# Kernel optimization log

Measured on AMD Instinct MI355X. Metric: run time of the kernel, lower is better.

The kernel has to match this reference:

```python
import jax, jax.numpy as jnp
import numpy as np

N_NODES = 50000
N_EDGES = 800000
IN_DIM = 13
HID = 64
LAYER_DIMS = [(IN_DIM, HID), (HID, HID), (HID, HID), (HID, HID), (HID, 1)]


def setup_inputs() -> dict:
    key = jax.random.key(0)
    ks = jax.random.split(key, 20)
    x = jax.random.normal(ks[0], (N_NODES, IN_DIM), dtype=jnp.float32)
    edge_index = jax.random.randint(ks[1], (2, N_EDGES), 0, N_NODES)
    edge_weight = jax.random.uniform(ks[2], (N_EDGES,), dtype=jnp.float32)
    inp = {"x": x, "edge_index": edge_index, "edge_weight": edge_weight}
    for i, (di, do) in enumerate(LAYER_DIMS):
        s = 1.0 / np.sqrt(di)
        inp[f"Wrel{i}"] = (jax.random.normal(ks[3 + 3 * i], (di, do)) * s).astype(jnp.float32)
        inp[f"brel{i}"] = jnp.zeros((do,), dtype=jnp.float32)
        inp[f"Wroot{i}"] = (jax.random.normal(ks[4 + 3 * i], (di, do)) * s).astype(jnp.float32)
    return inp


def _graph_conv(x, src, dst, ew, Wrel, brel, Wroot):
    # PyG GraphConv: out = lin_rel(sum_{j in N(i)} w_e * x_j) + lin_root(x_i)
    msgs = ew[:, None] * x[src]                      # [E, d_in] gather
    aggr = jax.ops.segment_sum(msgs, dst, num_segments=N_NODES)  # [N, d_in]
    return aggr @ Wrel + brel + x @ Wroot


def reference(x, edge_index, edge_weight,
              Wrel0, brel0, Wroot0,
              Wrel1, brel1, Wroot1,
              Wrel2, brel2, Wroot2,
              Wrel3, brel3, Wroot3,
              Wrel4, brel4, Wroot4):
    src, dst = edge_index[0], edge_index[1]  # source_to_target flow
    params = [
        (Wrel0, brel0, Wroot0),
        (Wrel1, brel1, Wroot1),
        (Wrel2, brel2, Wroot2),
        (Wrel3, brel3, Wroot3),
        (Wrel4, brel4, Wroot4),
    ]
    h = x
    for Wr, br, Ws in params[:-1]:
        h = jax.nn.relu(_graph_conv(h, src, dst, edge_weight, Wr, br, Ws))
    Wr, br, Ws = params[-1]
    h = _graph_conv(h, src, dst, edge_weight, Wr, br, Ws)
    return jax.nn.sigmoid(h)  # [N, 1]
```

## Files before the change

kernel.cpp:

```cpp
#include <hip/hip_runtime.h>
#include <math.h>

#define N_NODES 50000
#define N_EDGES 800000
#define NBUCKET 196
#define CHUNK 4096
#define NCHUNK 196
#define SCAN_N (NBUCKET * NCHUNK)
#define SB_A 151
#define SB_B 196
#define EPT 16
#define CAP_FINE 8192
#define MAXEPAD (N_EDGES + N_NODES * 4)

typedef __attribute__((ext_vector_type(8))) _Float16 f16x8;
typedef __attribute__((ext_vector_type(4))) float f32x4;

__device__ __forceinline__ int roundup4(int v) { return (v + 3) & ~3; }


__device__ __forceinline__ int block_excl_scan(int v, int* wsum) {
    int t = threadIdx.x, lane = t & 63, w = t >> 6;
    int sc = v;
    #pragma unroll
    for (int o = 1; o < 64; o <<= 1) {
        int u = __shfl_up(sc, o, 64);
        if (lane >= o) sc += u;
    }
    if (lane == 63) wsum[w] = sc;
    __syncthreads();
    int add = 0;
    #pragma unroll
    for (int j = 0; j < 4; ++j) if (j < w) add += wsum[j];
    return add + sc - v;
}


__global__ void hist_kernel(const int* __restrict__ dst, int* __restrict__ h,
                            int* __restrict__ counts) {
    __shared__ int hist[NBUCKET];
    for (int i = threadIdx.x; i < NBUCKET; i += 256) hist[i] = 0;
    __syncthreads();
    int base = blockIdx.x * CHUNK;
    int n = min(CHUNK, N_EDGES - base);
    for (int k = threadIdx.x; k < n; k += 256) {
        int d = dst[base + k];
        atomicAdd(&hist[d >> 8], 1);
        atomicAdd(&counts[d], 1);
    }
    __syncthreads();
    for (int i = threadIdx.x; i < NBUCKET; i += 256)
        h[i * NCHUNK + blockIdx.x] = hist[i];
}


__global__ void scan_blocks_dual(int* __restrict__ h, const int* __restrict__ counts,
                                 int* __restrict__ offs, int* __restrict__ blocksums) {
    __shared__ int wsum[4];
    int bid = blockIdx.x, t = threadIdx.x;
    if (bid < SB_A) {
        int i = bid * 256 + t;
        int v = (i < SCAN_N) ? h[i] : 0;
        int e = block_excl_scan(v, wsum);
        if (i < SCAN_N) h[i] = e;
        if (t == 255) blocksums[bid] = e + v;
    } else {
        int j = (bid - SB_A) * 256 + t;
        int v = (j < N_NODES) ? roundup4(counts[j]) : 0;
        int e = block_excl_scan(v, wsum);
        if (j < N_NODES) offs[j] = e;
        if (t == 255) blocksums[bid] = e + v;
    }
}

__global__ void scan_mid(const int* __restrict__ blocksums, int* __restrict__ blockoffs) {
    __shared__ int wsum[4];
    int base = (blockIdx.x == 0) ? 0 : SB_A;
    int n = (blockIdx.x == 0) ? SB_A : SB_B;
    int t = threadIdx.x;
    int v = (t < n) ? blocksums[base + t] : 0;
    int e = block_excl_scan(v, wsum);
    if (t < n) blockoffs[base + t] = e;
}

__global__ void scan_add_dual(int* __restrict__ h, int* __restrict__ offs,
                              const int* __restrict__ counts,
                              const int* __restrict__ blockoffs) {
    int bid = blockIdx.x, t = threadIdx.x;
    if (bid < SB_A) {
        int i = bid * 256 + t;
        if (i < SCAN_N) h[i] += blockoffs[bid];
    } else {
        int j = (bid - SB_A) * 256 + t;
        if (j < N_NODES) {
            int v = offs[j] + blockoffs[bid];
            offs[j] = v;
            if (j == N_NODES - 1) offs[N_NODES] = v + roundup4(counts[j]);
        }
    }
}


__launch_bounds__(256, 4)
__global__ void scatter_coarse(const int* __restrict__ src, const int* __restrict__ dst,
                               const float* __restrict__ ew, const int* __restrict__ hs,
                               int2* __restrict__ ecoarse) {
    __shared__ int cnt[NBUCKET];
    __shared__ int excl[NBUCKET];
    __shared__ int cur[NBUCKET];
    __shared__ int gbase[NBUCKET];
    __shared__ int wsum[4];
    __shared__ int2 stage[CHUNK];

    int t = threadIdx.x;
    int base = blockIdx.x * CHUNK;
    int n = min(CHUNK, N_EDGES - base);

    for (int i = t; i < NBUCKET; i += 256) {
        cnt[i] = 0;
        gbase[i] = hs[i * NCHUNK + blockIdx.x];
    }
    __syncthreads();

    int rx[EPT];
    float rw[EPT];
    #pragma unroll
    for (int j = 0; j < EPT; ++j) {
        int k = t + j * 256;
        if (k < n) {
            int e = base + k;
            int d = dst[e];
            rx[j] = (d << 16) | src[e];
            rw[j] = ew[e];
            atomicAdd(&cnt[d >> 8], 1);
        }
    }
    __syncthreads();

    {
        int v = (t < NBUCKET) ? cnt[t] : 0;
        int e = block_excl_scan(v, wsum);
        if (t < NBUCKET) { excl[t] = e; cur[t] = e; }
    }
    __syncthreads();

    #pragma unroll
    for (int j = 0; j < EPT; ++j) {
        int k = t + j * 256;
        if (k < n) {
            int b = ((unsigned)rx[j]) >> 24;
            int p = atomicAdd(&cur[b], 1);
            stage[p] = make_int2(rx[j], __float_as_int(rw[j]));
        }
    }
    __syncthreads();

    for (int k = t; k < n; k += 256) {
        int2 r = stage[k];
        int b = ((unsigned)r.x) >> 24;
        ecoarse[gbase[b] + (k - excl[b])] = r;
    }
}


__launch_bounds__(256)
__global__ void fine_sort(const int* __restrict__ h, const int* __restrict__ offs,
                          const int2* __restrict__ ecoarse, int2* __restrict__ esrt) {
    int b = blockIdx.x, t = threadIdx.x;
    __shared__ int cur[256];
    __shared__ int2 stage[CAP_FINE];
    int bstartU = h[b * NCHUNK];
    int bendU = (b == NBUCKET - 1) ? N_EDGES : h[(b + 1) * NCHUNK];
    int nbU = bendU - bstartU;
    int P = offs[b << 8];
    int nodeEnd = min((b + 1) << 8, N_NODES);
    int plen = offs[nodeEnd] - P;
    int dstv = (b << 8) + t;
    cur[t] = (dstv < N_NODES) ? offs[dstv] - P : 0;
    __syncthreads();
    if (plen <= CAP_FINE) {
        for (int k = t; k < plen; k += 256) stage[k] = make_int2(0, 0);
        __syncthreads();
        for (int k = t; k < nbU; k += 256) {
            int2 r = ecoarse[bstartU + k];
            int d = (((unsigned)r.x) >> 16) & 255;
            int p = atomicAdd(&cur[d], 1);
            stage[p] = make_int2(r.x & 0xFFFF, r.y);
        }
        __syncthreads();
        for (int k = t; k < plen; k += 256) esrt[P + k] = stage[k];
    } else {
        for (int k = t; k < plen; k += 256) esrt[P + k] = make_int2(0, 0);
        __syncthreads();
        for (int k = t; k < nbU; k += 256) {
            int2 r = ecoarse[bstartU + k];
            int d = (((unsigned)r.x) >> 16) & 255;
            int p = atomicAdd(&cur[d], 1);
            esrt[P + p] = make_int2(r.x & 0xFFFF, r.y);
        }
    }
}


__global__ void wconv(const float* __restrict__ W1r, const float* __restrict__ W1o,
                      const float* __restrict__ W2r, const float* __restrict__ W2o,
                      const float* __restrict__ W3r, const float* __restrict__ W3o,
                      _Float16* __restrict__ wfrag) {
    int b = blockIdx.x, t = threadIdx.x;
    const float* Wr = (b == 0) ? W1r : (b == 1) ? W2r : W3r;
    const float* Wo = (b == 0) ? W1o : (b == 1) ? W2o : W3o;
    _Float16* out = wfrag + (size_t)b * 8192;
    for (int i = t; i < 1024; i += 256) {
        int frag = i >> 6, lane = i & 63;
        int m = frag >> 3, ct = (frag >> 1) & 3, ks = frag & 1;
        int col = ct * 16 + (lane & 15);
        int kb = ks * 32 + (lane >> 4) * 8;
        const float* W = m ? Wo : Wr;
        f16x8 v;
        #pragma unroll
        for (int j = 0; j < 8; ++j) v[j] = (_Float16)W[(kb + j) * 64 + col];
        *(f16x8*)&out[(size_t)i * 8] = v;
    }
}


__device__ __forceinline__ float bcast(float v, int k) {
    return __int_as_float(__builtin_amdgcn_readlane(__float_as_int(v), k));
}


__launch_bounds__(256)
__global__ void layer0_fused(const int* __restrict__ offs, const int2* __restrict__ esrt,
                             const float* __restrict__ x, const float* __restrict__ Wrel,
                             const float* __restrict__ bias, const float* __restrict__ Wroot,
                             _Float16* __restrict__ h0) {
    int wid = (blockIdx.x * blockDim.x + threadIdx.x) >> 6;
    int lane = threadIdx.x & 63;
    float wr[13], wo[13];
    #pragma unroll
    for (int k = 0; k < 13; ++k) {
        wr[k] = Wrel[k * 64 + lane];
        wo[k] = Wroot[k * 64 + lane];
    }
    float bc = bias[lane];
    int q = lane >> 4, f = lane & 15;
    int beg = offs[wid], end = offs[wid + 1];
    float acc = 0.f;
    bool fv = (f < 13);
    int i = beg + q;
    for (; i + 4 < end; i += 8) {
        int2 e0 = esrt[i], e1 = esrt[i + 4];
        float v0 = fv ? x[(size_t)e0.x * 13 + f] : 0.f;
        float v1 = fv ? x[(size_t)e1.x * 13 + f] : 0.f;
        acc = fmaf(__int_as_float(e0.y), v0, acc);
        acc = fmaf(__int_as_float(e1.y), v1, acc);
    }
    if (i < end) {
        int2 e = esrt[i];
        float v = fv ? x[(size_t)e.x * 13 + f] : 0.f;
        acc = fmaf(__int_as_float(e.y), v, acc);
    }
    acc += __shfl_xor(acc, 16, 64);
    acc += __shfl_xor(acc, 32, 64);
    float hv = (lane < 13) ? x[(size_t)wid * 13 + lane] : 0.f;
    float a0 = bc, a1 = 0.f, a2 = 0.f, a3 = 0.f;
    #pragma unroll
    for (int k = 0; k + 2 <= 13; k += 2) {
        a0 = fmaf(bcast(acc, k), wr[k], a0);
        a1 = fmaf(bcast(hv, k), wo[k], a1);
        a2 = fmaf(bcast(acc, k + 1), wr[k + 1], a2);
        a3 = fmaf(bcast(hv, k + 1), wo[k + 1], a3);
    }
    a0 = fmaf(bcast(acc, 12), wr[12], a0);
    a1 = fmaf(bcast(hv, 12), wo[12], a1);
    float o = fmaxf((a0 + a2) + (a1 + a3), 0.f);
    h0[(size_t)wid * 64 + lane] = (_Float16)o;
}


template <bool FINAL>
__launch_bounds__(256)
__global__ void layer_fused(const int* __restrict__ offs, const int2* __restrict__ esrt,
                            const _Float16* __restrict__ hin, const _Float16* __restrict__ wfrag_l,
                            const float* __restrict__ bias, _Float16* __restrict__ hout,
                            const float* __restrict__ Wrel4, const float* __restrict__ Wroot4,
                            float* __restrict__ z, float* __restrict__ root) {
    __shared__ __align__(16) _Float16 bfrag[16][64][8];
    __shared__ __align__(16) float aggrT[32][68];
    __shared__ __align__(16) _Float16 hrootT[32][72];
    __shared__ float zpart[4][32], rpart[4][32];
    int t = threadIdx.x;
    int rowbase = blockIdx.x * 32;

    {
        const int4* s = (const int4*)wfrag_l;
        int4* d = (int4*)&bfrag[0][0][0];
        #pragma unroll
        for (int i = 0; i < 4; ++i) d[t + 256 * i] = s[t + 256 * i];
    }
    {
        int row = t >> 3, c8 = (t & 7) * 8;
        int gr = min(rowbase + row, N_NODES - 1);
        *(int4*)&hrootT[row][c8] = *(const int4*)&hin[(size_t)gr * 64 + c8];
    }

    int qw = t >> 4, l = t & 15;
    int hi8 = l >> 3, f8 = l & 7;
    #pragma unroll
    for (int rr = 0; rr < 2; ++rr) {
        int node = rowbase + qw + rr * 16;
        float a[8] = {0.f, 0.f, 0.f, 0.f, 0.f, 0.f, 0.f, 0.f};
        if (node < N_NODES) {
            int beg = offs[node], end = offs[node + 1];
            for (int i = beg; i < end; i += 4) {
                int4 p0 = *(const int4*)(esrt + i);
                int4 p1 = *(const int4*)(esrt + i + 2);
                int s0 = hi8 ? p0.z : p0.x;
                int s1 = hi8 ? p1.z : p1.x;
                float w0 = __int_as_float(hi8 ? p0.w : p0.y);
                float w1 = __int_as_float(hi8 ? p1.w : p1.y);
                f16x8 r0 = *(const f16x8*)(hin + (size_t)s0 * 64 + f8 * 8);
                f16x8 r1 = *(const f16x8*)(hin + (size_t)s1 * 64 + f8 * 8);
                #pragma unroll
                for (int j = 0; j < 8; ++j) {
                    a[j] = fmaf(w0, (float)r0[j], a[j]);
                    a[j] = fmaf(w1, (float)r1[j], a[j]);
                }
            }
        }
        #pragma unroll
        for (int j = 0; j < 8; ++j) a[j] += __shfl_xor(a[j], 8, 64);
        float4 wv = make_float4(a[hi8 * 4 + 0], a[hi8 * 4 + 1], a[hi8 * 4 + 2], a[hi8 * 4 + 3]);
        *(float4*)&aggrT[qw + rr * 16][f8 * 8 + hi8 * 4] = wv;
    }
    __syncthreads();

    int w = t >> 6, lane = t & 63;
    int r = lane & 15, koff = (lane >> 4) * 8;
    float bc = bias[w * 16 + r];
    float w4rv = 0.f, w4ov = 0.f;
    if (FINAL) { w4rv = Wrel4[w * 16 + r]; w4ov = Wroot4[w * 16 + r]; }

    #pragma unroll
    for (int g = 0; g < 2; ++g) {
        int lr = g * 16 + r;
        f16x8 Ah[2], Al[2], Ar[2];
        #pragma unroll
        for (int ks = 0; ks < 2; ++ks) {
            float4 a0 = *(const float4*)&aggrT[lr][ks * 32 + koff];
            float4 a1 = *(const float4*)&aggrT[lr][ks * 32 + koff + 4];
            float vv[8] = {a0.x, a0.y, a0.z, a0.w, a1.x, a1.y, a1.z, a1.w};
            f16x8 hi, lo;
            #pragma unroll
            for (int j = 0; j < 8; ++j) {
                _Float16 hh = (_Float16)vv[j];
                hi[j] = hh;
                lo[j] = (_Float16)(vv[j] - (float)hh);
            }
            Ah[ks] = hi;
            Al[ks] = lo;
            Ar[ks] = *(const f16x8*)&hrootT[lr][ks * 32 + koff];
        }
        f32x4 acc = {bc, bc, bc, bc};
        #pragma unroll
        for (int ks = 0; ks < 2; ++ks) {
            f16x8 br = *(const f16x8*)&bfrag[(0 * 4 + w) * 2 + ks][lane][0];
            f16x8 bo = *(const f16x8*)&bfrag[(1 * 4 + w) * 2 + ks][lane][0];
            acc = __builtin_amdgcn_mfma_f32_16x16x32_f16(Ah[ks], br, acc, 0, 0, 0);
            acc = __builtin_amdgcn_mfma_f32_16x16x32_f16(Al[ks], br, acc, 0, 0, 0);
            acc = __builtin_amdgcn_mfma_f32_16x16x32_f16(Ar[ks], bo, acc, 0, 0, 0);
        }
        if (FINAL) {
            #pragma unroll
            for (int j = 0; j < 4; ++j) {
                float o = fmaxf(acc[j], 0.f);
                float zz = o * w4rv, rv = o * w4ov;
                #pragma unroll
                for (int m = 1; m < 16; m <<= 1) {
                    zz += __shfl_xor(zz, m, 64);
                    rv += __shfl_xor(rv, m, 64);
                }
                if (r == 0) {
                    int lrow = g * 16 + (lane >> 4) * 4 + j;
                    zpart[w][lrow] = zz;
                    rpart[w][lrow] = rv;
                }
            }
        } else {
            #pragma unroll
            for (int j = 0; j < 4; ++j) {
                int row = rowbase + g * 16 + (lane >> 4) * 4 + j;
                if (row < N_NODES)
                    hout[(size_t)row * 64 + w * 16 + r] = (_Float16)fmaxf(acc[j], 0.f);
            }
        }
    }
    if (FINAL) {
        __syncthreads();
        if (t < 32) {
            int row = rowbase + t;
            if (row < N_NODES) {
                z[row] = zpart[0][t] + zpart[1][t] + zpart[2][t] + zpart[3][t];
                root[row] = rpart[0][t] + rpart[1][t] + rpart[2][t] + rpart[3][t];
            }
        }
    }
}


__launch_bounds__(256)
__global__ void final_aggr(const int* __restrict__ offs, const int2* __restrict__ esrt,
                           const float* __restrict__ z, const float* __restrict__ root,
                           const float* __restrict__ b4, float* __restrict__ out) {
    int tid = blockIdx.x * blockDim.x + threadIdx.x;
    int node = tid >> 2, g = tid & 3;
    if (node >= N_NODES) return;
    int beg = offs[node], end = offs[node + 1];
    float a = 0.f;
    int i = beg + g;
    for (; i + 4 < end; i += 8) {
        int2 e0 = esrt[i], e1 = esrt[i + 4];
        a = fmaf(__int_as_float(e0.y), z[e0.x], a);
        a = fmaf(__int_as_float(e1.y), z[e1.x], a);
    }
    if (i < end) {
        int2 e = esrt[i];
        a = fmaf(__int_as_float(e.y), z[e.x], a);
    }
    a += __shfl_xor(a, 1, 64);
    a += __shfl_xor(a, 2, 64);
    if (g == 0) {
        float v = a + b4[0] + root[node];
        out[node] = 1.f / (1.f + expf(-v));
    }
}


extern "C" void kernel_launch(void* const* d_in, const int* in_sizes, int n_in,
                              void* d_out, int out_size, void* d_ws, size_t ws_size,
                              hipStream_t stream) {
    const float* x = (const float*)d_in[0];
    const int* eidx = (const int*)d_in[1];
    const float* ew = (const float*)d_in[2];
    const float* Wrel[5];
    const float* brel[5];
    const float* Wroot[5];
    for (int i = 0; i < 5; ++i) {
        Wrel[i] = (const float*)d_in[3 + 3 * i];
        brel[i] = (const float*)d_in[4 + 3 * i];
        Wroot[i] = (const float*)d_in[5 + 3 * i];
    }
    const int* src = eidx;
    const int* dst = eidx + N_EDGES;
    float* out = (float*)d_out;

    char* ws = (char*)d_ws;
    size_t off = 0;
    auto alloc = [&](size_t bytes) -> void* {
        void* p = ws + off;
        off = (off + bytes + 255) & ~(size_t)255;
        return p;
    };
    int* h = (int*)alloc((size_t)(SCAN_N + 256) * 4);
    int* blocksums = (int*)alloc(512 * 4);
    int* blockoffs = (int*)alloc(512 * 4);
    int* counts = (int*)alloc((size_t)N_NODES * 4);
    int* offs = (int*)alloc((size_t)(N_NODES + 1) * 4);
    int2* esrt = (int2*)alloc((size_t)MAXEPAD * 8);
    _Float16* h0 = (_Float16*)alloc((size_t)N_NODES * 64 * 2);
    _Float16* h1 = (_Float16*)alloc((size_t)N_NODES * 64 * 2);
    _Float16* wfrag = (_Float16*)alloc((size_t)3 * 8192 * 2);
    float* z = (float*)alloc((size_t)N_NODES * 4);
    float* root = (float*)alloc((size_t)N_NODES * 4);
    int2* ecoarse = (int2*)h0;
    (void)ws_size; (void)in_sizes; (void)n_in; (void)out_size;

    hipMemsetAsync(counts, 0, (size_t)N_NODES * 4, stream);
    hist_kernel<<<NCHUNK, 256, 0, stream>>>(dst, h, counts);
    scan_blocks_dual<<<SB_A + SB_B, 256, 0, stream>>>(h, counts, offs, blocksums);
    scan_mid<<<2, 256, 0, stream>>>(blocksums, blockoffs);
    scan_add_dual<<<SB_A + SB_B, 256, 0, stream>>>(h, offs, counts, blockoffs);
    scatter_coarse<<<NCHUNK, 256, 0, stream>>>(src, dst, ew, h, ecoarse);
    fine_sort<<<NBUCKET, 256, 0, stream>>>(h, offs, ecoarse, esrt);

    wconv<<<3, 256, 0, stream>>>(Wrel[1], Wroot[1], Wrel[2], Wroot[2], Wrel[3], Wroot[3], wfrag);

    const int NODE_BLOCKS = N_NODES * 64 / 256;
    const int FB = (N_NODES + 31) / 32;

    layer0_fused<<<NODE_BLOCKS, 256, 0, stream>>>(offs, esrt, x, Wrel[0], brel[0], Wroot[0], h0);

    layer_fused<false><<<FB, 256, 0, stream>>>(offs, esrt, h0, wfrag, brel[1], h1,
                                               nullptr, nullptr, nullptr, nullptr);
    layer_fused<false><<<FB, 256, 0, stream>>>(offs, esrt, h1, wfrag + 8192, brel[2], h0,
                                               nullptr, nullptr, nullptr, nullptr);
    layer_fused<true><<<FB, 256, 0, stream>>>(offs, esrt, h0, wfrag + 16384, brel[3], nullptr,
                                              Wrel[4], Wroot[4], z, root);

    final_aggr<<<(N_NODES * 4 + 255) / 256, 256, 0, stream>>>(offs, esrt, z, root, brel[4], out);
}
```

Baseline: 193.3 us.

## Fold weight conversion into histogram kernel and cut LDS staging in layer kernels

Merges the fp16 weight-fragment conversion into the histogram kernel as extra blocks, removing one launch. In the fused layer kernel, MFMA B fragments are loaded directly into registers instead of being staged through shared memory, and the root rows are read from global memory rather than staged. The hi/lo fp16 split of the aggregate is done before the shared-memory store, which shrinks LDS usage, and the edge gather loop is unrolled to eight edges to expose more memory parallelism. The trade-offs are more registers per thread and repeated global reads of the weight fragments by every block.

```diff
diff --git a/kernel.cpp b/kernel.cpp
--- a/kernel.cpp
+++ b/kernel.cpp
@@ -37,7 +37,29 @@
 
 
 __global__ void hist_kernel(const int* __restrict__ dst, int* __restrict__ h,
-                            int* __restrict__ counts) {
+                            int* __restrict__ counts,
+                            const float* __restrict__ W1r, const float* __restrict__ W1o,
+                            const float* __restrict__ W2r, const float* __restrict__ W2o,
+                            const float* __restrict__ W3r, const float* __restrict__ W3o,
+                            _Float16* __restrict__ wfrag) {
+    if (blockIdx.x >= NCHUNK) {
+        int b = blockIdx.x - NCHUNK, t = threadIdx.x;
+        const float* Wr = (b == 0) ? W1r : (b == 1) ? W2r : W3r;
+        const float* Wo = (b == 0) ? W1o : (b == 1) ? W2o : W3o;
+        _Float16* out = wfrag + (size_t)b * 8192;
+        for (int i = t; i < 1024; i += 256) {
+            int frag = i >> 6, lane = i & 63;
+            int m = frag >> 3, ct = (frag >> 1) & 3, ks = frag & 1;
+            int col = ct * 16 + (lane & 15);
+            int kb = ks * 32 + (lane >> 4) * 8;
+            const float* W = m ? Wo : Wr;
+            f16x8 v;
+            #pragma unroll
+            for (int j = 0; j < 8; ++j) v[j] = (_Float16)W[(kb + j) * 64 + col];
+            *(f16x8*)&out[(size_t)i * 8] = v;
+        }
+        return;
+    }
     __shared__ int hist[NBUCKET];
     for (int i = threadIdx.x; i < NBUCKET; i += 256) hist[i] = 0;
     __syncthreads();
@@ -202,28 +224,6 @@
 }
 
 
-__global__ void wconv(const float* __restrict__ W1r, const float* __restrict__ W1o,
-                      const float* __restrict__ W2r, const float* __restrict__ W2o,
-                      const float* __restrict__ W3r, const float* __restrict__ W3o,
-                      _Float16* __restrict__ wfrag) {
-    int b = blockIdx.x, t = threadIdx.x;
-    const float* Wr = (b == 0) ? W1r : (b == 1) ? W2r : W3r;
-    const float* Wo = (b == 0) ? W1o : (b == 1) ? W2o : W3o;
-    _Float16* out = wfrag + (size_t)b * 8192;
-    for (int i = t; i < 1024; i += 256) {
-        int frag = i >> 6, lane = i & 63;
-        int m = frag >> 3, ct = (frag >> 1) & 3, ks = frag & 1;
-        int col = ct * 16 + (lane & 15);
-        int kb = ks * 32 + (lane >> 4) * 8;
-        const float* W = m ? Wo : Wr;
-        f16x8 v;
-        #pragma unroll
-        for (int j = 0; j < 8; ++j) v[j] = (_Float16)W[(kb + j) * 64 + col];
-        *(f16x8*)&out[(size_t)i * 8] = v;
-    }
-}
-
-
 __device__ __forceinline__ float bcast(float v, int k) {
     return __int_as_float(__builtin_amdgcn_readlane(__float_as_int(v), k));
 }
@@ -285,24 +285,21 @@
                             const float* __restrict__ bias, _Float16* __restrict__ hout,
                             const float* __restrict__ Wrel4, const float* __restrict__ Wroot4,
                             float* __restrict__ z, float* __restrict__ root) {
-    __shared__ __align__(16) _Float16 bfrag[16][64][8];
-    __shared__ __align__(16) float aggrT[32][68];
-    __shared__ __align__(16) _Float16 hrootT[32][72];
+    __shared__ __align__(16) _Float16 aggrHi[32][72];
+    __shared__ __align__(16) _Float16 aggrLo[32][72];
     __shared__ float zpart[4][32], rpart[4][32];
     int t = threadIdx.x;
     int rowbase = blockIdx.x * 32;
-
-    {
-        const int4* s = (const int4*)wfrag_l;
-        int4* d = (int4*)&bfrag[0][0][0];
-        #pragma unroll
-        for (int i = 0; i < 4; ++i) d[t + 256 * i] = s[t + 256 * i];
-    }
-    {
-        int row = t >> 3, c8 = (t & 7) * 8;
-        int gr = min(rowbase + row, N_NODES - 1);
-        *(int4*)&hrootT[row][c8] = *(const int4*)&hin[(size_t)gr * 64 + c8];
-    }
+    int w = t >> 6, lane = t & 63;
+
+    f16x8 br0 = *(const f16x8*)&wfrag_l[(size_t)(((0 * 4 + w) * 2 + 0) * 64 + lane) * 8];
+    f16x8 br1 = *(const f16x8*)&wfrag_l[(size_t)(((0 * 4 + w) * 2 + 1) * 64 + lane) * 8];
+    f16x8 bo0 = *(const f16x8*)&wfrag_l[(size_t)(((1 * 4 + w) * 2 + 0) * 64 + lane) * 8];
+    f16x8 bo1 = *(const f16x8*)&wfrag_l[(size_t)(((1 * 4 + w) * 2 + 1) * 64 + lane) * 8];
+    int r = lane & 15, kq = lane >> 4;
+    float bc = bias[w * 16 + r];
+    float w4rv = 0.f, w4ov = 0.f;
+    if (FINAL) { w4rv = Wrel4[w * 16 + r]; w4ov = Wroot4[w * 16 + r]; }
 
     int qw = t >> 4, l = t & 15;
     int hi8 = l >> 3, f8 = l & 7;
@@ -312,13 +309,33 @@
         float a[8] = {0.f, 0.f, 0.f, 0.f, 0.f, 0.f, 0.f, 0.f};
         if (node < N_NODES) {
             int beg = offs[node], end = offs[node + 1];
-            for (int i = beg; i < end; i += 4) {
+            int i = beg;
+            for (; i + 4 < end; i += 8) {
                 int4 p0 = *(const int4*)(esrt + i);
                 int4 p1 = *(const int4*)(esrt + i + 2);
-                int s0 = hi8 ? p0.z : p0.x;
-                int s1 = hi8 ? p1.z : p1.x;
-                float w0 = __int_as_float(hi8 ? p0.w : p0.y);
-                float w1 = __int_as_float(hi8 ? p1.w : p1.y);
+                int4 p2 = *(const int4*)(esrt + i + 4);
+                int4 p3 = *(const int4*)(esrt + i + 6);
+                int s0 = hi8 ? p0.z : p0.x; float w0 = __int_as_float(hi8 ? p0.w : p0.y);
+                int s1 = hi8 ? p1.z : p1.x; float w1 = __int_as_float(hi8 ? p1.w : p1.y);
+                int s2 = hi8 ? p2.z : p2.x; float w2 = __int_as_float(hi8 ? p2.w : p2.y);
+                int s3 = hi8 ? p3.z : p3.x; float w3 = __int_as_float(hi8 ? p3.w : p3.y);
+                f16x8 r0 = *(const f16x8*)(hin + (size_t)s0 * 64 + f8 * 8);
+                f16x8 r1 = *(const f16x8*)(hin + (size_t)s1 * 64 + f8 * 8);
+                f16x8 r2 = *(const f16x8*)(hin + (size_t)s2 * 64 + f8 * 8);
+                f16x8 r3 = *(const f16x8*)(hin + (size_t)s3 * 64 + f8 * 8);
+                #pragma unroll
+                for (int j = 0; j < 8; ++j) {
+                    a[j] = fmaf(w0, (float)r0[j], a[j]);
+                    a[j] = fmaf(w1, (float)r1[j], a[j]);
+                    a[j] = fmaf(w2, (float)r2[j], a[j]);
+                    a[j] = fmaf(w3, (float)r3[j], a[j]);
+                }
+            }
+            if (i < end) {
+                int4 p0 = *(const int4*)(esrt + i);
+                int4 p1 = *(const int4*)(esrt + i + 2);
+                int s0 = hi8 ? p0.z : p0.x; float w0 = __int_as_float(hi8 ? p0.w : p0.y);
+                int s1 = hi8 ? p1.z : p1.x; float w1 = __int_as_float(hi8 ? p1.w : p1.y);
                 f16x8 r0 = *(const f16x8*)(hin + (size_t)s0 * 64 + f8 * 8);
                 f16x8 r1 = *(const f16x8*)(hin + (size_t)s1 * 64 + f8 * 8);
                 #pragma unroll
@@ -330,45 +347,38 @@
         }
         #pragma unroll
         for (int j = 0; j < 8; ++j) a[j] += __shfl_xor(a[j], 8, 64);
-        float4 wv = make_float4(a[hi8 * 4 + 0], a[hi8 * 4 + 1], a[hi8 * 4 + 2], a[hi8 * 4 + 3]);
-        *(float4*)&aggrT[qw + rr * 16][f8 * 8 + hi8 * 4] = wv;
-    }
-    __syncthreads();
-
-    int w = t >> 6, lane = t & 63;
-    int r = lane & 15, koff = (lane >> 4) * 8;
-    float bc = bias[w * 16 + r];
-    float w4rv = 0.f, w4ov = 0.f;
-    if (FINAL) { w4rv = Wrel4[w * 16 + r]; w4ov = Wroot4[w * 16 + r]; }
+        f16x8 wv;
+        #pragma unroll
+        for (int j = 0; j < 8; ++j) {
+            _Float16 hh = (_Float16)a[j];
+            wv[j] = hi8 ? (_Float16)(a[j] - (float)hh) : hh;
+        }
+        int row = qw + rr * 16;
+        _Float16* dstp = hi8 ? &aggrLo[row][f8 * 8] : &aggrHi[row][f8 * 8];
+        *(f16x8*)dstp = wv;
+    }
+    __syncthreads();
 
     #pragma unroll
     for (int g = 0; g < 2; ++g) {
         int lr = g * 16 + r;
-        f16x8 Ah[2], Al[2], Ar[2];
-        #pragma unroll
-        for (int ks = 0; ks < 2; ++ks) {
-            float4 a0 = *(const float4*)&aggrT[lr][ks * 32 + koff];
-            float4 a1 = *(const float4*)&aggrT[lr][ks * 32 + koff + 4];
-            float vv[8] = {a0.x, a0.y, a0.z, a0.w, a1.x, a1.y, a1.z, a1.w};
-            f16x8 hi, lo;
-            #pragma unroll
-            for (int j = 0; j < 8; ++j) {
-                _Float16 hh = (_Float16)vv[j];
-                hi[j] = hh;
-                lo[j] = (_Float16)(vv[j] - (float)hh);
-            }
-            Ah[ks] = hi;
-            Al[ks] = lo;
-            Ar[ks] = *(const f16x8*)&hrootT[lr][ks * 32 + koff];
-        }
+        int grow = min(rowbase + lr, N_NODES - 1);
         f32x4 acc = {bc, bc, bc, bc};
-        #pragma unroll
-        for (int ks = 0; ks < 2; ++ks) {
-            f16x8 br = *(const f16x8*)&bfrag[(0 * 4 + w) * 2 + ks][lane][0];
-            f16x8 bo = *(const f16x8*)&bfrag[(1 * 4 + w) * 2 + ks][lane][0];
-            acc = __builtin_amdgcn_mfma_f32_16x16x32_f16(Ah[ks], br, acc, 0, 0, 0);
-            acc = __builtin_amdgcn_mfma_f32_16x16x32_f16(Al[ks], br, acc, 0, 0, 0);
-            acc = __builtin_amdgcn_mfma_f32_16x16x32_f16(Ar[ks], bo, acc, 0, 0, 0);
+        {
+            f16x8 Ah = *(const f16x8*)&aggrHi[lr][0 * 32 + kq * 8];
+            f16x8 Al = *(const f16x8*)&aggrLo[lr][0 * 32 + kq * 8];
+            f16x8 Ar = *(const f16x8*)&hin[(size_t)grow * 64 + 0 * 32 + kq * 8];
+            acc = __builtin_amdgcn_mfma_f32_16x16x32_f16(Ah, br0, acc, 0, 0, 0);
+            acc = __builtin_amdgcn_mfma_f32_16x16x32_f16(Al, br0, acc, 0, 0, 0);
+            acc = __builtin_amdgcn_mfma_f32_16x16x32_f16(Ar, bo0, acc, 0, 0, 0);
+        }
+        {
+            f16x8 Ah = *(const f16x8*)&aggrHi[lr][1 * 32 + kq * 8];
+            f16x8 Al = *(const f16x8*)&aggrLo[lr][1 * 32 + kq * 8];
+            f16x8 Ar = *(const f16x8*)&hin[(size_t)grow * 64 + 1 * 32 + kq * 8];
+            acc = __builtin_amdgcn_mfma_f32_16x16x32_f16(Ah, br1, acc, 0, 0, 0);
+            acc = __builtin_amdgcn_mfma_f32_16x16x32_f16(Al, br1, acc, 0, 0, 0);
+            acc = __builtin_amdgcn_mfma_f32_16x16x32_f16(Ar, bo1, acc, 0, 0, 0);
         }
         if (FINAL) {
             #pragma unroll
@@ -476,14 +486,14 @@
     (void)ws_size; (void)in_sizes; (void)n_in; (void)out_size;
 
     hipMemsetAsync(counts, 0, (size_t)N_NODES * 4, stream);
-    hist_kernel<<<NCHUNK, 256, 0, stream>>>(dst, h, counts);
+    hist_kernel<<<NCHUNK + 3, 256, 0, stream>>>(dst, h, counts,
+                                                Wrel[1], Wroot[1], Wrel[2], Wroot[2],
+                                                Wrel[3], Wroot[3], wfrag);
     scan_blocks_dual<<<SB_A + SB_B, 256, 0, stream>>>(h, counts, offs, blocksums);
     scan_mid<<<2, 256, 0, stream>>>(blocksums, blockoffs);
     scan_add_dual<<<SB_A + SB_B, 256, 0, stream>>>(h, offs, counts, blockoffs);
     scatter_coarse<<<NCHUNK, 256, 0, stream>>>(src, dst, ew, h, ecoarse);
     fine_sort<<<NBUCKET, 256, 0, stream>>>(h, offs, ecoarse, esrt);
-
-    wconv<<<3, 256, 0, stream>>>(Wrel[1], Wroot[1], Wrel[2], Wroot[2], Wrel[3], Wroot[3], wfrag);
 
     const int NODE_BLOCKS = N_NODES * 64 / 256;
     const int FB = (N_NODES + 31) / 32;
```

New measurement: 181.9 us. 5.9% less time.
